# Kernel optimization log

Hardware: AMD Instinct MI355X
Metric: run time of the kernel (lower is better)

The kernel has to match this reference:

```python
import jax, jax.numpy as jnp
import numpy as np

N = 2048
DIM = 1024
NH = 16
DK = DIM // NH  # 64

def setup_inputs() -> dict:
    key = jax.random.key(0)
    kx, kq, kk, kv = jax.random.split(key, 4)
    # nn.Linear(dim_in, dim_in, bias=False): init ~ U(-1/sqrt(dim_in), 1/sqrt(dim_in))
    b = 1.0 / np.sqrt(DIM)
    return {
        "x": jax.random.normal(kx, (N, DIM), dtype=jnp.float32),
        "rela": jnp.zeros((1,), dtype=jnp.float32),  # unused by the module
        "Wq": jax.random.uniform(kq, (DIM, DIM), jnp.float32, -b, b),
        "Wk": jax.random.uniform(kk, (DIM, DIM), jnp.float32, -b, b),
        "Wv": jax.random.uniform(kv, (DIM, DIM), jnp.float32, -b, b),
    }

def reference(x, rela, Wq, Wk, Wv):
    n = x.shape[0]
    scale = 1.0 / np.sqrt(DK)
    # torch Linear: x @ W.T ; reshape to [n, nh, dk] then heads first -> [nh, n, dk]
    q = (x @ Wq.T).reshape(n, NH, DK).transpose(1, 0, 2)
    k = (x @ Wk.T).reshape(n, NH, DK).transpose(1, 0, 2)
    v = (x @ Wv.T).reshape(n, NH, DK).transpose(1, 0, 2)
    dist = jnp.einsum('hnd,hmd->hnm', q, k) * scale  # [nh, n, n]
    dist = jax.nn.softmax(dist, axis=-1)
    att = jnp.einsum('hnm,hmd->hnd', dist, v)        # [nh, n, dk]
    return att.transpose(1, 0, 2).reshape(n, DIM)
```

## Files before the change

kernel.cpp:

```cpp
#include <hip/hip_runtime.h>

#define SN 2048
#define SDIM 1024
#define SNH 16
#define SDK 64
#define NZ 4

typedef short short8 __attribute__((ext_vector_type(8)));
typedef short s16x4 __attribute__((ext_vector_type(4)));
typedef unsigned short u16;
typedef u16 u16x4 __attribute__((ext_vector_type(4)));
typedef u16 u16x8 __attribute__((ext_vector_type(8)));
typedef unsigned u32x4 __attribute__((ext_vector_type(4)));
typedef float f32x4 __attribute__((ext_vector_type(4)));

__device__ __forceinline__ u16 f2b(float f){
  unsigned u = __builtin_bit_cast(unsigned, f);
  u += 0x7fffu + ((u >> 16) & 1u);
  return (u16)(u >> 16);
}

__device__ __forceinline__ float b2f(u16 b){
  unsigned u = ((unsigned)b) << 16;
  return __builtin_bit_cast(float, u);
}

__device__ __forceinline__ float fast_exp2(float x){
#if __has_builtin(__builtin_amdgcn_exp2f)
  return __builtin_amdgcn_exp2f(x);
#else
  float r; asm("v_exp_f32 %0, %1" : "=v"(r) : "v"(x)); return r;
#endif
}

__device__ __forceinline__ unsigned packbf(float lo, float hi){
  unsigned a = __builtin_bit_cast(unsigned, lo);
  unsigned b = __builtin_bit_cast(unsigned, hi);
#if __has_builtin(__builtin_amdgcn_perm)
  return __builtin_amdgcn_perm(b, a, 0x07060302u);
#else
  return (a >> 16) | (b & 0xffff0000u);
#endif
}

__device__ __forceinline__ void async_cp16(const void* g, void* l){
  __builtin_amdgcn_global_load_lds(
      (const __attribute__((address_space(1))) unsigned*)g,
      (__attribute__((address_space(3))) unsigned*)l, 16, 0, 0);
}

__global__ void conv_all(const float* __restrict__ x, const float* __restrict__ wq,
                         const float* __restrict__ wk, const float* __restrict__ wv,
                         u16* __restrict__ xb, u16* __restrict__ wb){
  const int NX4 = (SN * SDIM) / 4;
  const int NW4 = (SDIM * SDIM) / 4;
  const int total = NX4 + 3 * NW4;
  int i = blockIdx.x * blockDim.x + threadIdx.x;
  int stride = gridDim.x * blockDim.x;
  for (int idx = i; idx < total; idx += stride){
    const float* src; u16* dst; int off;
    if (idx < NX4){ src = x; dst = xb; off = idx; }
    else {
      int t = idx - NX4; int ws = t >> 18; off = t & (NW4 - 1);
      src = (ws == 0) ? wq : ((ws == 1) ? wk : wv);
      dst = wb + (size_t)ws * SDIM * SDIM;
    }
    float4 v = reinterpret_cast<const float4*>(src)[off];
    u16x4 o = { f2b(v.x), f2b(v.y), f2b(v.z), f2b(v.w) };
    *reinterpret_cast<u16x4*>(&dst[(size_t)off * 4]) = o;
  }
}

__global__ __launch_bounds__(512, 6) void proj_gemm(const u16* __restrict__ xb, const u16* __restrict__ wb,
                                                    u16* __restrict__ qb, u16* __restrict__ kb,
                                                    u16* __restrict__ vtb){
  __shared__ __align__(16) u16 Asm[2][64 * 64];
  __shared__ __align__(16) u16 Bsm[2][128 * 64];
  const int tid = threadIdx.x, w = tid >> 6, lane = tid & 63;
  const int r = lane & 15, hi = lane >> 4;
  const int tm = blockIdx.x * 64, tn = blockIdx.y * 128;
  const int z = blockIdx.z;
  const u16* W = wb + (size_t)z * SDIM * SDIM;
  const int kk = w >> 2;
  const int wr = (w >> 1) & 1, wc = w & 1;
  const int srow = lane >> 3;
  const int schunk = (lane & 7) ^ (lane >> 3);
  f32x4 acc[2][4] = {};

  auto stage = [&](int b, int kt){
    async_cp16(xb + (size_t)(tm + w * 8 + srow) * SDIM + kt + schunk * 8, &Asm[b][w * 8 * 64]);
#pragma unroll
    for (int c = 0; c < 2; c++){
      int row = w * 16 + c * 8;
      async_cp16(W + (size_t)(tn + row + srow) * SDIM + kt + schunk * 8, &Bsm[b][row * 64]);
    }
  };

  stage(0, 0);
  asm volatile("s_waitcnt vmcnt(0)" ::: "memory");
  __builtin_amdgcn_s_barrier();
  __builtin_amdgcn_sched_barrier(0);

  int cur = 0;
  for (int kt = 0; kt < SDIM; kt += 64){
    if (kt + 64 < SDIM) stage(cur ^ 1, kt + 64);
    __builtin_amdgcn_s_setprio(1);
    {
      short8 af[2], bf[4];
      int cc = (kk * 4 + hi) ^ (r & 7);
#pragma unroll
      for (int mr = 0; mr < 2; mr++)
        af[mr] = *reinterpret_cast<const short8*>(&Asm[cur][(wr * 32 + mr * 16 + r) * 64 + cc * 8]);
#pragma unroll
      for (int nr = 0; nr < 4; nr++)
        bf[nr] = *reinterpret_cast<const short8*>(&Bsm[cur][(wc * 64 + nr * 16 + r) * 64 + cc * 8]);
#pragma unroll
      for (int mr = 0; mr < 2; mr++)
#pragma unroll
        for (int nr = 0; nr < 4; nr++)
          acc[mr][nr] = __builtin_amdgcn_mfma_f32_16x16x32_bf16(af[mr], bf[nr], acc[mr][nr], 0, 0, 0);
    }
    __builtin_amdgcn_s_setprio(0);
    asm volatile("s_waitcnt vmcnt(0)" ::: "memory");
    __builtin_amdgcn_s_barrier();
    __builtin_amdgcn_sched_barrier(0);
    cur ^= 1;
  }

  float* scr = reinterpret_cast<float*>(&Bsm[0][0]);
  const int slot = w & 3;
  if (kk == 1){
#pragma unroll
    for (int mr = 0; mr < 2; mr++)
#pragma unroll
      for (int nr = 0; nr < 4; nr++){
        int fid = mr * 4 + nr;
        int a = slot * 2048 + fid * 256 + r * 16 + ((hi + r) & 3) * 4;
        *reinterpret_cast<f32x4*>(&scr[a]) = acc[mr][nr];
      }
  }
  __syncthreads();
  if (kk == 0){
#pragma unroll
    for (int mr = 0; mr < 2; mr++)
#pragma unroll
      for (int nr = 0; nr < 4; nr++){
        int fid = mr * 4 + nr;
        int a = slot * 2048 + fid * 256 + r * 16 + ((hi + r) & 3) * 4;
        f32x4 t = *reinterpret_cast<const f32x4*>(&scr[a]);
        acc[mr][nr][0] += t[0]; acc[mr][nr][1] += t[1];
        acc[mr][nr][2] += t[2]; acc[mr][nr][3] += t[3];
      }

    if (z == 2){
#pragma unroll
      for (int mr = 0; mr < 2; mr++)
#pragma unroll
        for (int nr = 0; nr < 4; nr++){
          u16x4 o4 = { f2b(acc[mr][nr][0]), f2b(acc[mr][nr][1]),
                       f2b(acc[mr][nr][2]), f2b(acc[mr][nr][3]) };
          int col = tn + wc * 64 + nr * 16 + r;
          int row = tm + wr * 32 + mr * 16 + hi * 4;
          *reinterpret_cast<u16x4*>(&vtb[(size_t)col * SN + row]) = o4;
        }
    } else {
      u16* outp = (z == 0) ? qb : kb;
      const float scl = (z == 0) ? 0.18033688011112043f : 1.0f;
#pragma unroll
      for (int mr = 0; mr < 2; mr++)
#pragma unroll
        for (int nr = 0; nr < 4; nr++)
#pragma unroll
          for (int j = 0; j < 4; j++){
            int row = tm + wr * 32 + mr * 16 + hi * 4 + j;
            int col = tn + wc * 64 + nr * 16 + r;
            outp[(size_t)row * SDIM + col] = f2b(acc[mr][nr][j] * scl);
          }
    }
  }
}

__global__ __launch_bounds__(256, 4) void attn(const u16* __restrict__ qb, const u16* __restrict__ kb,
                                               const u16* __restrict__ vtb,
                                               u16* __restrict__ po, float* __restrict__ pl){
  __shared__ __align__(16) u16 klds[2][64 * 64];
  __shared__ __align__(16) u16 vlds[2][64 * 64];
  const int tid = threadIdx.x, w = tid >> 6, lane = tid & 63;
  const int r = lane & 15, hi = lane >> 4;

  int flat = blockIdx.x + 16 * blockIdx.y + 256 * blockIdx.z;
  int sw = (flat & 7) * 128 + (flat >> 3);
  const int q0 = (sw & 15) * 128, h = (sw >> 4) & 15, z = sw >> 8;

  const int srow_off = lane >> 3;
  const int schunk   = (lane & 7) ^ (lane >> 3);

  short8 aq[2][2];
#pragma unroll
  for (int sub = 0; sub < 2; sub++){
    int qrow = q0 + w * 32 + sub * 16 + r;
    aq[sub][0] = *reinterpret_cast<const short8*>(&qb[(size_t)qrow * SDIM + h * SDK + hi * 8]);
    aq[sub][1] = *reinterpret_cast<const short8*>(&qb[(size_t)qrow * SDIM + h * SDK + 32 + hi * 8]);
  }
  f32x4 oacc[2][4] = {};
  float lacc0 = 0.f, lacc1 = 0.f;
  short8 paf0[2], paf1[2];

  auto stageK = [&](int buf, int t){
#pragma unroll
    for (int c = 0; c < 2; c++){
      int rho = w * 16 + c * 8 + srow_off;
      int kvp = 32 * (rho >> 5) + 8 * ((rho >> 2) & 3) + 4 * ((rho >> 4) & 1) + (rho & 3);
      async_cp16(kb + (size_t)(t + kvp) * SDIM + h * SDK + schunk * 8,
                 &klds[buf][(w * 16 + c * 8) * 64]);
    }
  };
  auto stageV = [&](int buf, int t){
#pragma unroll
    for (int c = 0; c < 2; c++){
      int rho = w * 16 + c * 8 + srow_off;
      async_cp16(vtb + (size_t)(h * SDK + rho) * SN + t + schunk * 8,
                 &vlds[buf][(w * 16 + c * 8) * 64]);
    }
  };

  auto QK = [&](const u16* kbuf, f32x4* s0, f32x4* s1){
    __builtin_amdgcn_s_setprio(1);
#pragma unroll
    for (int ct = 0; ct < 4; ct++){
      int row = ct * 16 + r;
      int c0 = hi ^ (r & 7);
      short8 bk0 = *reinterpret_cast<const short8*>(&kbuf[row * 64 + c0 * 8]);
      short8 bk1 = *reinterpret_cast<const short8*>(&kbuf[row * 64 + (c0 ^ 4) * 8]);
      f32x4 zero = {};
      s0[ct] = __builtin_amdgcn_mfma_f32_16x16x32_bf16(bk0, aq[0][0], zero, 0, 0, 0);
      s1[ct] = __builtin_amdgcn_mfma_f32_16x16x32_bf16(bk0, aq[1][0], zero, 0, 0, 0);
      s0[ct] = __builtin_amdgcn_mfma_f32_16x16x32_bf16(bk1, aq[0][1], s0[ct], 0, 0, 0);
      s1[ct] = __builtin_amdgcn_mfma_f32_16x16x32_bf16(bk1, aq[1][1], s1[ct], 0, 0, 0);
    }
    __builtin_amdgcn_s_setprio(0);
  };

  auto EXPPACK = [&](const f32x4* s0, const f32x4* s1){
    uint2 pc0[4], pc1[4];
#pragma unroll
    for (int ct = 0; ct < 4; ct++){
      float a0 = fast_exp2(s0[ct][0]), a1 = fast_exp2(s0[ct][1]);
      float a2 = fast_exp2(s0[ct][2]), a3 = fast_exp2(s0[ct][3]);
      lacc0 += (a0 + a1) + (a2 + a3);
      pc0[ct].x = packbf(a0, a1);
      pc0[ct].y = packbf(a2, a3);
      float b0 = fast_exp2(s1[ct][0]), b1 = fast_exp2(s1[ct][1]);
      float b2 = fast_exp2(s1[ct][2]), b3 = fast_exp2(s1[ct][3]);
      lacc1 += (b0 + b1) + (b2 + b3);
      pc1[ct].x = packbf(b0, b1);
      pc1[ct].y = packbf(b2, b3);
    }
#pragma unroll
    for (int c = 0; c < 2; c++){
      u32x4 u0 = { pc0[2*c].x, pc0[2*c].y, pc0[2*c+1].x, pc0[2*c+1].y };
      u32x4 u1 = { pc1[2*c].x, pc1[2*c].y, pc1[2*c+1].x, pc1[2*c+1].y };
      paf0[c] = __builtin_bit_cast(short8, u0);
      paf1[c] = __builtin_bit_cast(short8, u1);
    }
  };

  auto PV = [&](const u16* vbuf){
    __builtin_amdgcn_s_setprio(1);
#pragma unroll
    for (int dt = 0; dt < 4; dt++){
      int row = dt * 16 + r;
      int swz = row & 7;
      short8 bvc[2];
#pragma unroll
      for (int c = 0; c < 2; c++)
        bvc[c] = *reinterpret_cast<const short8*>(&vbuf[row * 64 + ((4 * c + hi) ^ swz) * 8]);
#pragma unroll
      for (int c = 0; c < 2; c++){
        oacc[0][dt] = __builtin_amdgcn_mfma_f32_16x16x32_bf16(paf0[c], bvc[c], oacc[0][dt], 0, 0, 0);
        oacc[1][dt] = __builtin_amdgcn_mfma_f32_16x16x32_bf16(paf1[c], bvc[c], oacc[1][dt], 0, 0, 0);
      }
    }
    __builtin_amdgcn_s_setprio(0);
  };

  const int t0 = z * (SN / 4);
  const int NT = (SN / 4) / 64;

  stageK(0, t0); stageV(0, t0); stageK(1, t0 + 64);
  asm volatile("s_waitcnt vmcnt(0)" ::: "memory");
  __builtin_amdgcn_s_barrier();
  __builtin_amdgcn_sched_barrier(0);
  {
    f32x4 s0[4], s1[4];
    QK(&klds[0][0], s0, s1);
    EXPPACK(s0, s1);
  }
  __builtin_amdgcn_s_barrier();
  __builtin_amdgcn_sched_barrier(0);

  for (int it = 0; it < NT; ++it){
    const int cur = it & 1;
    const int t = t0 + it * 64;
    const bool hasN1 = (it + 1 < NT), hasN2 = (it + 2 < NT);
    if (hasN1) stageV(cur ^ 1, t + 64);
    if (hasN2) stageK(cur, t + 128);
    f32x4 s0[4], s1[4];
    if (hasN1) QK(&klds[cur ^ 1][0], s0, s1);
    PV(&vlds[cur][0]);
    if (hasN1) EXPPACK(s0, s1);
    asm volatile("s_waitcnt vmcnt(0)" ::: "memory");
    __builtin_amdgcn_s_barrier();
    __builtin_amdgcn_sched_barrier(0);
  }

  lacc0 += __shfl_xor(lacc0, 16); lacc0 += __shfl_xor(lacc0, 32);
  lacc1 += __shfl_xor(lacc1, 16); lacc1 += __shfl_xor(lacc1, 32);

  const size_t zh = (size_t)z * SNH + h;
#pragma unroll
  for (int sub = 0; sub < 2; sub++)
#pragma unroll
    for (int dt = 0; dt < 4; dt++)
#pragma unroll
      for (int j = 0; j < 4; j++){
        int row = q0 + w * 32 + sub * 16 + hi * 4 + j;
        po[(zh * SN + row) * SDK + dt * 16 + r] = f2b(oacc[sub][dt][j]);
      }
  if (hi == 0){
    pl[zh * SN + q0 + w * 32 + r] = lacc0;
    pl[zh * SN + q0 + w * 32 + 16 + r] = lacc1;
  }
}

__global__ void merge(const u16* __restrict__ po, const float* __restrict__ pl,
                      float* __restrict__ out){
  int gid = blockIdx.x * blockDim.x + threadIdx.x;
  int c8 = gid & 7;
  int rowid = gid >> 3;
  int h = rowid & 15, q = rowid >> 4;
  float L = 0.f;
  float o[8] = {};
#pragma unroll
  for (int z = 0; z < NZ; z++){
    size_t zh = (size_t)z * SNH + h;
    L += pl[zh * SN + q];
    u16x8 a = *reinterpret_cast<const u16x8*>(&po[(zh * SN + q) * SDK + c8 * 8]);
#pragma unroll
    for (int e = 0; e < 8; e++) o[e] += b2f(a[e]);
  }
  float rL = 1.0f / L;
  float4 o0 = { o[0] * rL, o[1] * rL, o[2] * rL, o[3] * rL };
  float4 o1 = { o[4] * rL, o[5] * rL, o[6] * rL, o[7] * rL };
  float* dst = &out[(size_t)q * SDIM + h * SDK + c8 * 8];
  *reinterpret_cast<float4*>(dst) = o0;
  *reinterpret_cast<float4*>(dst + 4) = o1;
}

extern "C" void kernel_launch(void* const* d_in, const int* in_sizes, int n_in,
                              void* d_out, int out_size, void* d_ws, size_t ws_size,
                              hipStream_t stream){
  const float* x  = (const float*)d_in[0];
  const float* Wq = (const float*)d_in[2];
  const float* Wk = (const float*)d_in[3];
  const float* Wv = (const float*)d_in[4];
  float* out = (float*)d_out;

  char* ws = (char*)d_ws;
  u16* xb  = (u16*)(ws);
  u16* wb  = (u16*)(ws + (4  << 20));
  u16* qb  = (u16*)(ws + (10 << 20));
  u16* kb  = (u16*)(ws + (14 << 20));
  u16* vtb = (u16*)(ws + (18 << 20));
  u16* po  = (u16*)(ws + (22 << 20));
  float* pl = (float*)(ws + (38 << 20));

  conv_all<<<2048, 256, 0, stream>>>(x, Wq, Wk, Wv, xb, wb);

  dim3 pg(SN / 64, SDIM / 128, 3);
  proj_gemm<<<pg, 512, 0, stream>>>(xb, wb, qb, kb, vtb);

  dim3 ag(SN / 128, SNH, NZ);
  attn<<<ag, 256, 0, stream>>>(qb, kb, vtb, po, pl);

  merge<<<(SN * SNH * 8) / 256, 256, 0, stream>>>(po, pl, out);
}
```

Before: 59.97 us.

## Load K/V fragments directly from global in attention, swizzle projection block order

The attention kernel drops its LDS double-buffered async staging of K and V tiles and barriers. Each wave now loads its MFMA fragments straight from global memory into registers every iteration, relying on L2/cache for reuse across waves. The projection GEMM also remaps block indices so consecutive blocks share tiles for better L2 locality. Removing LDS and barriers may raise occupancy, but the attention loop loses prefetch overlap and duplicates global loads across the four waves.

```diff
diff --git a/kernel.cpp b/kernel.cpp
--- a/kernel.cpp
+++ b/kernel.cpp
@@ -7,7 +7,6 @@
 #define NZ 4
 
 typedef short short8 __attribute__((ext_vector_type(8)));
-typedef short s16x4 __attribute__((ext_vector_type(4)));
 typedef unsigned short u16;
 typedef u16 u16x4 __attribute__((ext_vector_type(4)));
 typedef u16 u16x8 __attribute__((ext_vector_type(8)));
@@ -78,8 +77,13 @@
   __shared__ __align__(16) u16 Bsm[2][128 * 64];
   const int tid = threadIdx.x, w = tid >> 6, lane = tid & 63;
   const int r = lane & 15, hi = lane >> 4;
-  const int tm = blockIdx.x * 64, tn = blockIdx.y * 128;
-  const int z = blockIdx.z;
+
+  int flat = blockIdx.x + 32 * blockIdx.y + 256 * blockIdx.z;
+  int sw = (flat & 7) * 96 + (flat >> 3);
+  const int tm = (sw & 31) * 64;
+  const int tn = ((sw >> 5) & 7) * 128;
+  const int z = sw >> 8;
+
   const u16* W = wb + (size_t)z * SDIM * SDIM;
   const int kk = w >> 2;
   const int wr = (w >> 1) & 1, wc = w & 1;
@@ -180,20 +184,15 @@
   }
 }
 
-__global__ __launch_bounds__(256, 4) void attn(const u16* __restrict__ qb, const u16* __restrict__ kb,
-                                               const u16* __restrict__ vtb,
-                                               u16* __restrict__ po, float* __restrict__ pl){
-  __shared__ __align__(16) u16 klds[2][64 * 64];
-  __shared__ __align__(16) u16 vlds[2][64 * 64];
+__global__ __launch_bounds__(256) void attn(const u16* __restrict__ qb, const u16* __restrict__ kb,
+                                            const u16* __restrict__ vtb,
+                                            u16* __restrict__ po, float* __restrict__ pl){
   const int tid = threadIdx.x, w = tid >> 6, lane = tid & 63;
   const int r = lane & 15, hi = lane >> 4;
 
   int flat = blockIdx.x + 16 * blockIdx.y + 256 * blockIdx.z;
   int sw = (flat & 7) * 128 + (flat >> 3);
   const int q0 = (sw & 15) * 128, h = (sw >> 4) & 15, z = sw >> 8;
-
-  const int srow_off = lane >> 3;
-  const int schunk   = (lane & 7) ^ (lane >> 3);
 
   short8 aq[2][2];
 #pragma unroll
@@ -204,114 +203,79 @@
   }
   f32x4 oacc[2][4] = {};
   float lacc0 = 0.f, lacc1 = 0.f;
-  short8 paf0[2], paf1[2];
-
-  auto stageK = [&](int buf, int t){
-#pragma unroll
-    for (int c = 0; c < 2; c++){
-      int rho = w * 16 + c * 8 + srow_off;
-      int kvp = 32 * (rho >> 5) + 8 * ((rho >> 2) & 3) + 4 * ((rho >> 4) & 1) + (rho & 3);
-      async_cp16(kb + (size_t)(t + kvp) * SDIM + h * SDK + schunk * 8,
-                 &klds[buf][(w * 16 + c * 8) * 64]);
-    }
-  };
-  auto stageV = [&](int buf, int t){
-#pragma unroll
-    for (int c = 0; c < 2; c++){
-      int rho = w * 16 + c * 8 + srow_off;
-      async_cp16(vtb + (size_t)(h * SDK + rho) * SN + t + schunk * 8,
-                 &vlds[buf][(w * 16 + c * 8) * 64]);
-    }
-  };
-
-  auto QK = [&](const u16* kbuf, f32x4* s0, f32x4* s1){
-    __builtin_amdgcn_s_setprio(1);
-#pragma unroll
-    for (int ct = 0; ct < 4; ct++){
-      int row = ct * 16 + r;
-      int c0 = hi ^ (r & 7);
-      short8 bk0 = *reinterpret_cast<const short8*>(&kbuf[row * 64 + c0 * 8]);
-      short8 bk1 = *reinterpret_cast<const short8*>(&kbuf[row * 64 + (c0 ^ 4) * 8]);
-      f32x4 zero = {};
-      s0[ct] = __builtin_amdgcn_mfma_f32_16x16x32_bf16(bk0, aq[0][0], zero, 0, 0, 0);
-      s1[ct] = __builtin_amdgcn_mfma_f32_16x16x32_bf16(bk0, aq[1][0], zero, 0, 0, 0);
-      s0[ct] = __builtin_amdgcn_mfma_f32_16x16x32_bf16(bk1, aq[0][1], s0[ct], 0, 0, 0);
-      s1[ct] = __builtin_amdgcn_mfma_f32_16x16x32_bf16(bk1, aq[1][1], s1[ct], 0, 0, 0);
-    }
-    __builtin_amdgcn_s_setprio(0);
-  };
-
-  auto EXPPACK = [&](const f32x4* s0, const f32x4* s1){
-    uint2 pc0[4], pc1[4];
-#pragma unroll
-    for (int ct = 0; ct < 4; ct++){
-      float a0 = fast_exp2(s0[ct][0]), a1 = fast_exp2(s0[ct][1]);
-      float a2 = fast_exp2(s0[ct][2]), a3 = fast_exp2(s0[ct][3]);
-      lacc0 += (a0 + a1) + (a2 + a3);
-      pc0[ct].x = packbf(a0, a1);
-      pc0[ct].y = packbf(a2, a3);
-      float b0 = fast_exp2(s1[ct][0]), b1 = fast_exp2(s1[ct][1]);
-      float b2 = fast_exp2(s1[ct][2]), b3 = fast_exp2(s1[ct][3]);
-      lacc1 += (b0 + b1) + (b2 + b3);
-      pc1[ct].x = packbf(b0, b1);
-      pc1[ct].y = packbf(b2, b3);
-    }
-#pragma unroll
-    for (int c = 0; c < 2; c++){
-      u32x4 u0 = { pc0[2*c].x, pc0[2*c].y, pc0[2*c+1].x, pc0[2*c+1].y };
-      u32x4 u1 = { pc1[2*c].x, pc1[2*c].y, pc1[2*c+1].x, pc1[2*c+1].y };
-      paf0[c] = __builtin_bit_cast(short8, u0);
-      paf1[c] = __builtin_bit_cast(short8, u1);
-    }
-  };
-
-  auto PV = [&](const u16* vbuf){
-    __builtin_amdgcn_s_setprio(1);
-#pragma unroll
-    for (int dt = 0; dt < 4; dt++){
-      int row = dt * 16 + r;
-      int swz = row & 7;
-      short8 bvc[2];
-#pragma unroll
-      for (int c = 0; c < 2; c++)
-        bvc[c] = *reinterpret_cast<const short8*>(&vbuf[row * 64 + ((4 * c + hi) ^ swz) * 8]);
-#pragma unroll
-      for (int c = 0; c < 2; c++){
-        oacc[0][dt] = __builtin_amdgcn_mfma_f32_16x16x32_bf16(paf0[c], bvc[c], oacc[0][dt], 0, 0, 0);
-        oacc[1][dt] = __builtin_amdgcn_mfma_f32_16x16x32_bf16(paf1[c], bvc[c], oacc[1][dt], 0, 0, 0);
-      }
-    }
-    __builtin_amdgcn_s_setprio(0);
-  };
+
+  const int kvbase = 8 * (r >> 2) + (r & 3);
 
   const int t0 = z * (SN / 4);
   const int NT = (SN / 4) / 64;
 
-  stageK(0, t0); stageV(0, t0); stageK(1, t0 + 64);
-  asm volatile("s_waitcnt vmcnt(0)" ::: "memory");
-  __builtin_amdgcn_s_barrier();
-  __builtin_amdgcn_sched_barrier(0);
-  {
+  for (int it = 0; it < NT; ++it){
+    const int t = t0 + it * 64;
+
+    short8 bk[4][2];
+#pragma unroll
+    for (int ct = 0; ct < 4; ct++){
+      int kv = t + 32 * (ct >> 1) + 4 * (ct & 1) + kvbase;
+      const u16* kp = kb + (size_t)kv * SDIM + h * SDK + hi * 8;
+      bk[ct][0] = *reinterpret_cast<const short8*>(kp);
+      bk[ct][1] = *reinterpret_cast<const short8*>(kp + 32);
+    }
+
     f32x4 s0[4], s1[4];
-    QK(&klds[0][0], s0, s1);
-    EXPPACK(s0, s1);
-  }
-  __builtin_amdgcn_s_barrier();
-  __builtin_amdgcn_sched_barrier(0);
-
-  for (int it = 0; it < NT; ++it){
-    const int cur = it & 1;
-    const int t = t0 + it * 64;
-    const bool hasN1 = (it + 1 < NT), hasN2 = (it + 2 < NT);
-    if (hasN1) stageV(cur ^ 1, t + 64);
-    if (hasN2) stageK(cur, t + 128);
-    f32x4 s0[4], s1[4];
-    if (hasN1) QK(&klds[cur ^ 1][0], s0, s1);
-    PV(&vlds[cur][0]);
-    if (hasN1) EXPPACK(s0, s1);
-    asm volatile("s_waitcnt vmcnt(0)" ::: "memory");
-    __builtin_amdgcn_s_barrier();
-    __builtin_amdgcn_sched_barrier(0);
+    __builtin_amdgcn_s_setprio(1);
+#pragma unroll
+    for (int ct = 0; ct < 4; ct++){
+      f32x4 zero = {};
+      s0[ct] = __builtin_amdgcn_mfma_f32_16x16x32_bf16(bk[ct][0], aq[0][0], zero, 0, 0, 0);
+      s1[ct] = __builtin_amdgcn_mfma_f32_16x16x32_bf16(bk[ct][0], aq[1][0], zero, 0, 0, 0);
+      s0[ct] = __builtin_amdgcn_mfma_f32_16x16x32_bf16(bk[ct][1], aq[0][1], s0[ct], 0, 0, 0);
+      s1[ct] = __builtin_amdgcn_mfma_f32_16x16x32_bf16(bk[ct][1], aq[1][1], s1[ct], 0, 0, 0);
+    }
+    __builtin_amdgcn_s_setprio(0);
+
+    short8 bv[4][2];
+#pragma unroll
+    for (int dt = 0; dt < 4; dt++){
+      const u16* vp = vtb + (size_t)(h * SDK + dt * 16 + r) * SN + t + hi * 8;
+      bv[dt][0] = *reinterpret_cast<const short8*>(vp);
+      bv[dt][1] = *reinterpret_cast<const short8*>(vp + 32);
+    }
+
+    short8 paf0[2], paf1[2];
+    {
+      uint2 pc0[4], pc1[4];
+#pragma unroll
+      for (int ct = 0; ct < 4; ct++){
+        float a0 = fast_exp2(s0[ct][0]), a1 = fast_exp2(s0[ct][1]);
+        float a2 = fast_exp2(s0[ct][2]), a3 = fast_exp2(s0[ct][3]);
+        lacc0 += (a0 + a1) + (a2 + a3);
+        pc0[ct].x = packbf(a0, a1);
+        pc0[ct].y = packbf(a2, a3);
+        float b0 = fast_exp2(s1[ct][0]), b1 = fast_exp2(s1[ct][1]);
+        float b2 = fast_exp2(s1[ct][2]), b3 = fast_exp2(s1[ct][3]);
+        lacc1 += (b0 + b1) + (b2 + b3);
+        pc1[ct].x = packbf(b0, b1);
+        pc1[ct].y = packbf(b2, b3);
+      }
+#pragma unroll
+      for (int c = 0; c < 2; c++){
+        u32x4 u0 = { pc0[2*c].x, pc0[2*c].y, pc0[2*c+1].x, pc0[2*c+1].y };
+        u32x4 u1 = { pc1[2*c].x, pc1[2*c].y, pc1[2*c+1].x, pc1[2*c+1].y };
+        paf0[c] = __builtin_bit_cast(short8, u0);
+        paf1[c] = __builtin_bit_cast(short8, u1);
+      }
+    }
+
+    __builtin_amdgcn_s_setprio(1);
+#pragma unroll
+    for (int dt = 0; dt < 4; dt++){
+#pragma unroll
+      for (int c = 0; c < 2; c++){
+        oacc[0][dt] = __builtin_amdgcn_mfma_f32_16x16x32_bf16(paf0[c], bv[dt][c], oacc[0][dt], 0, 0, 0);
+        oacc[1][dt] = __builtin_amdgcn_mfma_f32_16x16x32_bf16(paf1[c], bv[dt][c], oacc[1][dt], 0, 0, 0);
+      }
+    }
+    __builtin_amdgcn_s_setprio(0);
   }
 
   lacc0 += __shfl_xor(lacc0, 16); lacc0 += __shfl_xor(lacc0, 32);
```

Result: slower. 102.7 us (+71.2%).
